# Performance work log

Measured on AMD Instinct MI355X. Metric: run time of the kernel, lower is better.

The kernel has to match this reference:

```python
import jax, jax.numpy as jnp
import numpy as np

INF = 1.0e10


def _embed(x, W1, b1, W2, b2):
    # TemplateAngleEmbedder: Linear -> GELU -> Linear
    return jax.nn.gelu(x @ W1 + b1) @ W2 + b2


def setup_inputs() -> dict:
    key = jax.random.key(0)
    ks = jax.random.split(key, 12)
    B, N, K = 2, 768, 30
    d_pair, d_msa, relpos_k = 128, 256, 32
    num_bins = 2 * relpos_k + 1  # 65
    s = 0.02
    # valid rigid frames: random rotations via QR (det fixed to +1) + translations
    A = jax.random.normal(ks[0], (B, N, 3, 3), dtype=jnp.float32)
    Q, _ = jnp.linalg.qr(A)
    Q = Q * jnp.sign(jnp.linalg.det(Q))[..., None, None]
    t = jax.random.normal(ks[1], (B, N, 3), dtype=jnp.float32) * 10.0
    frames = (jnp.zeros((B, N, 4, 4), dtype=jnp.float32)
              .at[..., :3, :3].set(Q)
              .at[..., :3, 3].set(t)
              .at[..., 3, 3].set(1.0))
    residue_index = jnp.tile(jnp.arange(N, dtype=jnp.int32)[None], (B, 1))
    return {
        'tf': jax.random.normal(ks[2], (B, N, 1), dtype=jnp.float32),
        'residue_index': residue_index,
        'true_frame_tensor': frames,
        'seq_mask': jnp.ones((B, N), dtype=jnp.float32),
        'W_tf': jax.random.normal(ks[3], (1, d_msa), dtype=jnp.float32) * s,
        'b_tf': jnp.zeros((d_msa,), dtype=jnp.float32),
        'Wa1': jax.random.normal(ks[4], (5, d_pair), dtype=jnp.float32) * s,
        'ba1': jnp.zeros((d_pair,), dtype=jnp.float32),
        'Wa2': jax.random.normal(ks[5], (d_pair, d_pair), dtype=jnp.float32) * s,
        'ba2': jnp.zeros((d_pair,), dtype=jnp.float32),
        'Wd1': jax.random.normal(ks[6], (3, d_pair), dtype=jnp.float32) * s,
        'bd1': jnp.zeros((d_pair,), dtype=jnp.float32),
        'Wd2': jax.random.normal(ks[7], (d_pair, d_pair), dtype=jnp.float32) * s,
        'bd2': jnp.zeros((d_pair,), dtype=jnp.float32),
        'W_rp': jax.random.normal(ks[8], (num_bins, d_pair), dtype=jnp.float32) * s,
        'b_rp': jnp.zeros((d_pair,), dtype=jnp.float32),
        'topk': 30,
    }


def _pair_features(true_frame_tensor, residue_index, seq_mask, topk):
    # get_pair_info: pairwise dist + masked topk KNN + gather + frame decompose
    B, N = residue_index.shape
    R = true_frame_tensor[..., :3, :3]          # [B,N,3,3]
    t = true_frame_tensor[..., :3, 3]           # [B,N,3]
    xyz = t[:, None, :, :] - t[:, :, None, :]   # [B,i,j,3] = t_j - t_i
    dist = jnp.linalg.norm(xyz, axis=-1)        # [B,N,N]
    eye = jnp.eye(N, dtype=bool)[None]          # [1,N,N]
    smask = seq_mask.astype(bool)
    pair_mask = smask[:, None, :] & smask[:, :, None]
    rel = residue_index[:, None, :] - residue_index[:, :, None]
    connect = jnp.abs(rel) == 1
    d4topk = jnp.where(eye, INF, dist)
    d4topk = jnp.where(pair_mask, d4topk, INF)
    d4topk = jnp.where(connect, -INF, d4topk)
    _, idx = jax.lax.top_k(-d4topk, topk)       # k smallest -> [B,N,K]
    topk_dist = jnp.take_along_axis(dist, idx, axis=-1)          # [B,N,K]
    knn_mask = jnp.take_along_axis(pair_mask & ~eye, idx, axis=-1)
    # gather neighbor frames and decompose into frame i's local coordinates:
    # t_rel = R_i^T (t_j - t_i)
    bidx = jnp.arange(B)[:, None, None]
    tj = t[bidx, idx]                            # [B,N,K,3]
    t_rel = jnp.einsum('bnxy,bnkx->bnky', R, tj - t[:, :, None, :])
    d = topk_dist[..., None]
    direct_angle = jnp.where(d > 0, t_rel / jnp.where(d > 0, d, 1.0), 0.0)
    eye_g = jnp.take_along_axis(jnp.broadcast_to(eye, (B, N, N)), idx, axis=-1)
    conn_g = jnp.take_along_axis(connect, idx, axis=-1)
    f32 = topk_dist.dtype
    ang_in = jnp.concatenate([eye_g[..., None].astype(f32),
                              conn_g[..., None].astype(f32),
                              direct_angle], axis=-1)            # [B,N,K,5]
    dst_in = jnp.concatenate([eye_g[..., None].astype(f32),
                              conn_g[..., None].astype(f32),
                              topk_dist[..., None]], axis=-1)    # [B,N,K,3]
    return ang_in, dst_in, knn_mask


def reference(tf, residue_index, true_frame_tensor, seq_mask,
              W_tf, b_tf, Wa1, ba1, Wa2, ba2, Wd1, bd1, Wd2, bd2,
              W_rp, b_rp, topk):
    relpos_k = (W_rp.shape[0] - 1) // 2
    # pair info computed under no_grad in the original
    ang_in, dst_in, _ = jax.lax.stop_gradient(
        _pair_features(true_frame_tensor, residue_index, seq_mask, topk))
    # tf is replaced by ones in the original forward
    ones_tf = jnp.ones_like(tf[..., :1])
    s = ones_tf @ W_tf + b_tf                                   # [B,N,d_msa]
    pair_rep_angle = _embed(ang_in, Wa1, ba1, Wa2, ba2)         # [B,N,K,d_pair]
    pair_rep_dist = _embed(dst_in, Wd1, bd1, Wd2, bd2)          # [B,N,K,d_pair]
    # relpos embedding (use_chain_relative=False)
    rp = residue_index[:, :, None] - residue_index[:, None, :]
    rp = jnp.clip(rp, -relpos_k, relpos_k) + relpos_k
    oh = jax.nn.one_hot(rp, W_rp.shape[0], dtype=W_rp.dtype)    # [B,N,N,65]
    relpos_emb = oh @ W_rp + b_rp                               # [B,N,N,d_pair]
    return (s, pair_rep_angle, pair_rep_dist, relpos_emb)
```

## Files before the change

kernel.cpp:

```cpp
#include <hip/hip_runtime.h>

typedef unsigned short u16;
typedef unsigned int   u32;
typedef unsigned long long u64;

typedef __attribute__((ext_vector_type(8))) short  short8;
typedef __attribute__((ext_vector_type(4))) float  floatx4;

__device__ __forceinline__ u16 f2bf(float f) {
    u32 u = __float_as_uint(f);
    u32 r = (u + 0x7FFFu + ((u >> 16) & 1u)) >> 16;
    return (u16)r;
}
__device__ __forceinline__ float bfu2f(u16 u) {
    union { u32 i; float f; } v; v.i = ((u32)u) << 16; return v.f;
}

constexpr int N     = 768;
constexpr int TOPK  = 30;
constexpr long OFF_ANG = 393216;
constexpr long OFF_DST = 6291456;
constexpr long OFF_RP  = 12189696;

__device__ __forceinline__ float dist_f32(float dx, float dy, float dz) {
    float s = __fadd_rn(__fadd_rn(__fmul_rn(dx, dx), __fmul_rn(dy, dy)), __fmul_rn(dz, dz));
    return __fsqrt_rn(s);
}

__global__ __launch_bounds__(256) void topk_feat_kernel(
    const float* __restrict__ frames, const int* __restrict__ resi,
    const float* __restrict__ smask, float* __restrict__ feat)
{
    __shared__ float s_t[N * 3];
    __shared__ float s_m[N];
    __shared__ int   s_r[N];
    int tid = threadIdx.x;
    int r0  = blockIdx.x * 4;
    int b   = r0 / N;
    for (int j = tid; j < N; j += 256) {
        s_r[j] = resi[b * N + j];
        s_m[j] = smask[b * N + j];
        long fb = (long)(b * N + j) * 16;
        s_t[j * 3 + 0] = frames[fb + 0 * 4 + 3];
        s_t[j * 3 + 1] = frames[fb + 1 * 4 + 3];
        s_t[j * 3 + 2] = frames[fb + 2 * 4 + 3];
    }
    __syncthreads();

    int wave = tid >> 6, lane = tid & 63;
    int r = r0 + wave;
    int i = r - b * N;
    float ti0 = s_t[i * 3], ti1 = s_t[i * 3 + 1], ti2 = s_t[i * 3 + 2];
    float mi = s_m[i];
    int   ri = s_r[i];

    u64 keys[12];
#pragma unroll
    for (int c = 0; c < 12; c++) {
        int j = lane + 64 * c;
        float dx = __fadd_rn(s_t[j * 3 + 0], -ti0);
        float dy = __fadd_rn(s_t[j * 3 + 1], -ti1);
        float dz = __fadd_rn(s_t[j * 3 + 2], -ti2);
        float dist = dist_f32(dx, dy, dz);
        int rd = s_r[j] - ri;
        bool conn = (rd == 1) || (rd == -1);
        bool bad  = (j == i) || (mi == 0.f) || (s_m[j] == 0.f);
        float d4 = conn ? -1e10f : (bad ? 1e10f : dist);
        u32 u = __float_as_uint(d4);
        u32 su = (u >> 31) ? ~u : (u | 0x80000000u);
        keys[c] = ((u64)su << 32) | (u32)j;
    }

    int my_j = 0;
    for (int k = 0; k < TOPK; k++) {
        u64 m = keys[0];
#pragma unroll
        for (int c = 1; c < 12; c++) m = m < keys[c] ? m : keys[c];
#pragma unroll
        for (int off = 32; off >= 1; off >>= 1) {
            u32 lo = (u32)m, hi = (u32)(m >> 32);
            u32 lo2 = __shfl_xor(lo, off);
            u32 hi2 = __shfl_xor(hi, off);
            u64 o = ((u64)hi2 << 32) | lo2;
            m = m < o ? m : o;
        }
#pragma unroll
        for (int c = 0; c < 12; c++) keys[c] = (keys[c] == m) ? ~0ull : keys[c];
        if (lane == k) my_j = (int)(m & 0xffffffffu);
    }

    if (lane < TOPK) {
        int j = my_j;
        float dx = __fadd_rn(s_t[j * 3 + 0], -ti0);
        float dy = __fadd_rn(s_t[j * 3 + 1], -ti1);
        float dz = __fadd_rn(s_t[j * 3 + 2], -ti2);
        float dist = dist_f32(dx, dy, dz);
        long fb = (long)(b * N + i) * 16;
        float R00 = frames[fb + 0], R01 = frames[fb + 1], R02 = frames[fb + 2];
        float R10 = frames[fb + 4], R11 = frames[fb + 5], R12 = frames[fb + 6];
        float R20 = frames[fb + 8], R21 = frames[fb + 9], R22 = frames[fb + 10];
        float t0 = R00 * dx + R10 * dy + R20 * dz;
        float t1 = R01 * dx + R11 * dy + R21 * dz;
        float t2 = R02 * dx + R12 * dy + R22 * dz;
        float a0 = dist > 0.f ? t0 / dist : 0.f;
        float a1 = dist > 0.f ? t1 / dist : 0.f;
        float a2 = dist > 0.f ? t2 / dist : 0.f;
        int rd = s_r[j] - ri;
        float conn = ((rd == 1) || (rd == -1)) ? 1.f : 0.f;
        float eye  = (j == i) ? 1.f : 0.f;
        long base = ((long)r * TOPK + lane) * 8;
        feat[base + 0] = eye; feat[base + 1] = conn;
        feat[base + 2] = a0;  feat[base + 3] = a1; feat[base + 4] = a2;
        feat[base + 5] = eye; feat[base + 6] = conn; feat[base + 7] = dist;
    }
}

template<int NF, int FOFF>
__device__ __forceinline__ void embed_body(
    int blk, const float* __restrict__ feat,
    const float* __restrict__ W1, const float* __restrict__ b1,
    const float* __restrict__ W2, const float* __restrict__ b2,
    float* __restrict__ out,
    u16* s_w2h, u16* s_w2l, float* s_w1, float* s_b1, float* s_b2)
{
    int tid = threadIdx.x;
    for (int e = tid; e < 128 * 128; e += 256) {
        int kk = e >> 7, nn = e & 127;
        float w  = W2[e];
        u16 hi = f2bf(w);
        float lo = __fadd_rn(w, -bfu2f(hi));
        s_w2h[nn * 136 + kk] = hi;
        s_w2l[nn * 136 + kk] = f2bf(lo);
    }
    for (int e = tid; e < NF * 128; e += 256) s_w1[e] = W1[e];
    if (tid < 128) { s_b1[tid] = b1[tid]; s_b2[tid] = b2[tid]; }
    __syncthreads();

    int wave = tid >> 6, lane = tid & 63;
    int m = lane & 15, q = lane >> 4;
    int row0 = blk * 64 + wave * 16;
    int row  = row0 + m;

    float f[NF];
#pragma unroll
    for (int t = 0; t < NF; t++) f[t] = feat[(long)row * 8 + FOFF + t];

    floatx4 acc[8];
#pragma unroll
    for (int nt = 0; nt < 8; nt++) acc[nt] = (floatx4){0.f, 0.f, 0.f, 0.f};

#pragma unroll
    for (int s = 0; s < 4; s++) {
        short8 ahi, alo;
#pragma unroll
        for (int jj = 0; jj < 8; jj++) {
            int kk = 32 * s + 8 * q + jj;
            float h = s_b1[kk];
#pragma unroll
            for (int t = 0; t < NF; t++) h += f[t] * s_w1[t * 128 + kk];
            float u  = 0.7978845608028654f * (h + 0.044715f * h * h * h);
            float e2 = __expf(-2.f * fabsf(u));
            float th = (1.f - e2) / (1.f + e2);
            th = u < 0.f ? -th : th;
            float g = 0.5f * h * (1.f + th);
            u16 ghi = f2bf(g);
            float glo = __fadd_rn(g, -bfu2f(ghi));
            ahi[jj] = (short)ghi;
            alo[jj] = (short)f2bf(glo);
        }
#pragma unroll
        for (int nt = 0; nt < 8; nt++) {
            int boff = (nt * 16 + m) * 136 + 32 * s + 8 * q;
            short8 bh = *(const short8*)&s_w2h[boff];
            short8 bl = *(const short8*)&s_w2l[boff];
            acc[nt] = __builtin_amdgcn_mfma_f32_16x16x32_bf16(ahi, bh, acc[nt], 0, 0, 0);
            acc[nt] = __builtin_amdgcn_mfma_f32_16x16x32_bf16(alo, bh, acc[nt], 0, 0, 0);
            acc[nt] = __builtin_amdgcn_mfma_f32_16x16x32_bf16(ahi, bl, acc[nt], 0, 0, 0);
        }
    }

#pragma unroll
    for (int nt = 0; nt < 8; nt++) {
#pragma unroll
        for (int rg = 0; rg < 4; rg++) {
            int rr = row0 + q * 4 + rg;
            int cc = nt * 16 + m;
            out[(long)rr * 128 + cc] = acc[nt][rg] + s_b2[cc];
        }
    }
}

__global__ __launch_bounds__(256) void fused_embed_s_kernel(
    const float* __restrict__ feat,
    const float* __restrict__ Wa1, const float* __restrict__ ba1,
    const float* __restrict__ Wa2, const float* __restrict__ ba2,
    const float* __restrict__ Wd1, const float* __restrict__ bd1,
    const float* __restrict__ Wd2, const float* __restrict__ bd2,
    const float* __restrict__ W_tf, const float* __restrict__ b_tf,
    float* __restrict__ out)
{
    __shared__ __align__(16) u16 s_w2h[128 * 136];
    __shared__ __align__(16) u16 s_w2l[128 * 136];
    __shared__ float s_w1[5 * 128];
    __shared__ float s_b1[128];
    __shared__ float s_b2[128];
    unsigned bx = blockIdx.x;
    if (bx < 720) {
        embed_body<5, 0>(bx, feat, Wa1, ba1, Wa2, ba2, out + OFF_ANG,
                         s_w2h, s_w2l, s_w1, s_b1, s_b2);
    } else if (bx < 1440) {
        embed_body<3, 5>(bx - 720, feat, Wd1, bd1, Wd2, bd2, out + OFF_DST,
                         s_w2h, s_w2l, s_w1, s_b1, s_b2);
    } else {
        int gid = (bx - 1440) * 256 + threadIdx.x;
        int c0  = (gid * 4) & 255;
        floatx4 o;
        o.x = W_tf[c0 + 0] + b_tf[c0 + 0];
        o.y = W_tf[c0 + 1] + b_tf[c0 + 1];
        o.z = W_tf[c0 + 2] + b_tf[c0 + 2];
        o.w = W_tf[c0 + 3] + b_tf[c0 + 3];
        *((floatx4*)out + gid) = o;
    }
}

__global__ __launch_bounds__(256) void relpos_kernel(
    const int* __restrict__ resi,
    const float* __restrict__ W_rp, const float* __restrict__ b_rp,
    float* __restrict__ out)
{
    int v   = blockIdx.x * 256 + threadIdx.x;
    int row = v >> 5, seg = v & 31;
    int b   = row >= N * N ? 1 : 0;
    int rem = row - b * (N * N);
    int i   = rem / N;
    int j   = rem - i * N;
    int d   = resi[b * N + i] - resi[b * N + j];
    d = d < -32 ? -32 : (d > 32 ? 32 : d);
    int bin = d + 32;
    floatx4 w  = ((const floatx4*)(W_rp + bin * 128))[seg];
    floatx4 bb = ((const floatx4*)b_rp)[seg];
    floatx4 o = w + bb;
    ((floatx4*)(out + OFF_RP))[v] = o;
}

extern "C" void kernel_launch(void* const* d_in, const int* in_sizes, int n_in,
                              void* d_out, int out_size, void* d_ws, size_t ws_size,
                              hipStream_t stream) {
    const int*   resi   = (const int*)d_in[1];
    const float* frames = (const float*)d_in[2];
    const float* smask  = (const float*)d_in[3];
    const float* W_tf   = (const float*)d_in[4];
    const float* b_tf   = (const float*)d_in[5];
    const float* Wa1    = (const float*)d_in[6];
    const float* ba1    = (const float*)d_in[7];
    const float* Wa2    = (const float*)d_in[8];
    const float* ba2    = (const float*)d_in[9];
    const float* Wd1    = (const float*)d_in[10];
    const float* bd1    = (const float*)d_in[11];
    const float* Wd2    = (const float*)d_in[12];
    const float* bd2    = (const float*)d_in[13];
    const float* W_rp   = (const float*)d_in[14];
    const float* b_rp   = (const float*)d_in[15];
    float* out  = (float*)d_out;
    float* feat = (float*)d_ws;

    hipLaunchKernelGGL(topk_feat_kernel, dim3(384), dim3(256), 0, stream,
                       frames, resi, smask, feat);
    hipLaunchKernelGGL(fused_embed_s_kernel, dim3(1824), dim3(256), 0, stream,
                       feat, Wa1, ba1, Wa2, ba2, Wd1, bd1, Wd2, bd2,
                       W_tf, b_tf, out);
    hipLaunchKernelGGL(relpos_kernel, dim3(147456), dim3(256), 0, stream,
                       resi, W_rp, b_rp, out);
}
```

Measured before the change: 717.7 us.

## Fuse relpos write into topk kernel with shared-memory bias-folded table

Merges the relpos embedding into the top-k feature kernel. The extra 1152 blocks each stage W_rp+b_rp and residue indices in shared memory, then stream 128 float4 writes per thread, replacing a 147456-block launch that read global weights per element. The relpos stores can overlap with the latency-bound top-k work and one launch is dropped. In exchange, shared memory per block grows to about 36KB for all blocks, which may lower occupancy of the top-k blocks.

```diff
diff --git a/kernel.cpp b/kernel.cpp
--- a/kernel.cpp
+++ b/kernel.cpp
@@ -27,91 +27,124 @@
     return __fsqrt_rn(s);
 }
 
-__global__ __launch_bounds__(256) void topk_feat_kernel(
+__global__ __launch_bounds__(256) void topk_relpos_kernel(
     const float* __restrict__ frames, const int* __restrict__ resi,
-    const float* __restrict__ smask, float* __restrict__ feat)
+    const float* __restrict__ smask, float* __restrict__ feat,
+    const float* __restrict__ W_rp, const float* __restrict__ b_rp,
+    float* __restrict__ out)
 {
-    __shared__ float s_t[N * 3];
-    __shared__ float s_m[N];
-    __shared__ int   s_r[N];
+    __shared__ __align__(16) char smem_raw[65 * 128 * 4 + N * 4];
     int tid = threadIdx.x;
-    int r0  = blockIdx.x * 4;
-    int b   = r0 / N;
-    for (int j = tid; j < N; j += 256) {
-        s_r[j] = resi[b * N + j];
-        s_m[j] = smask[b * N + j];
-        long fb = (long)(b * N + j) * 16;
-        s_t[j * 3 + 0] = frames[fb + 0 * 4 + 3];
-        s_t[j * 3 + 1] = frames[fb + 1 * 4 + 3];
-        s_t[j * 3 + 2] = frames[fb + 2 * 4 + 3];
-    }
-    __syncthreads();
-
-    int wave = tid >> 6, lane = tid & 63;
-    int r = r0 + wave;
-    int i = r - b * N;
-    float ti0 = s_t[i * 3], ti1 = s_t[i * 3 + 1], ti2 = s_t[i * 3 + 2];
-    float mi = s_m[i];
-    int   ri = s_r[i];
-
-    u64 keys[12];
-#pragma unroll
-    for (int c = 0; c < 12; c++) {
-        int j = lane + 64 * c;
-        float dx = __fadd_rn(s_t[j * 3 + 0], -ti0);
-        float dy = __fadd_rn(s_t[j * 3 + 1], -ti1);
-        float dz = __fadd_rn(s_t[j * 3 + 2], -ti2);
-        float dist = dist_f32(dx, dy, dz);
-        int rd = s_r[j] - ri;
-        bool conn = (rd == 1) || (rd == -1);
-        bool bad  = (j == i) || (mi == 0.f) || (s_m[j] == 0.f);
-        float d4 = conn ? -1e10f : (bad ? 1e10f : dist);
-        u32 u = __float_as_uint(d4);
-        u32 su = (u >> 31) ? ~u : (u | 0x80000000u);
-        keys[c] = ((u64)su << 32) | (u32)j;
-    }
-
-    int my_j = 0;
-    for (int k = 0; k < TOPK; k++) {
-        u64 m = keys[0];
-#pragma unroll
-        for (int c = 1; c < 12; c++) m = m < keys[c] ? m : keys[c];
-#pragma unroll
-        for (int off = 32; off >= 1; off >>= 1) {
-            u32 lo = (u32)m, hi = (u32)(m >> 32);
-            u32 lo2 = __shfl_xor(lo, off);
-            u32 hi2 = __shfl_xor(hi, off);
-            u64 o = ((u64)hi2 << 32) | lo2;
-            m = m < o ? m : o;
-        }
-#pragma unroll
-        for (int c = 0; c < 12; c++) keys[c] = (keys[c] == m) ? ~0ull : keys[c];
-        if (lane == k) my_j = (int)(m & 0xffffffffu);
-    }
-
-    if (lane < TOPK) {
-        int j = my_j;
-        float dx = __fadd_rn(s_t[j * 3 + 0], -ti0);
-        float dy = __fadd_rn(s_t[j * 3 + 1], -ti1);
-        float dz = __fadd_rn(s_t[j * 3 + 2], -ti2);
-        float dist = dist_f32(dx, dy, dz);
-        long fb = (long)(b * N + i) * 16;
-        float R00 = frames[fb + 0], R01 = frames[fb + 1], R02 = frames[fb + 2];
-        float R10 = frames[fb + 4], R11 = frames[fb + 5], R12 = frames[fb + 6];
-        float R20 = frames[fb + 8], R21 = frames[fb + 9], R22 = frames[fb + 10];
-        float t0 = R00 * dx + R10 * dy + R20 * dz;
-        float t1 = R01 * dx + R11 * dy + R21 * dz;
-        float t2 = R02 * dx + R12 * dy + R22 * dz;
-        float a0 = dist > 0.f ? t0 / dist : 0.f;
-        float a1 = dist > 0.f ? t1 / dist : 0.f;
-        float a2 = dist > 0.f ? t2 / dist : 0.f;
-        int rd = s_r[j] - ri;
-        float conn = ((rd == 1) || (rd == -1)) ? 1.f : 0.f;
-        float eye  = (j == i) ? 1.f : 0.f;
-        long base = ((long)r * TOPK + lane) * 8;
-        feat[base + 0] = eye; feat[base + 1] = conn;
-        feat[base + 2] = a0;  feat[base + 3] = a1; feat[base + 4] = a2;
-        feat[base + 5] = eye; feat[base + 6] = conn; feat[base + 7] = dist;
+
+    if (blockIdx.x < 384) {
+        float* s_t = (float*)smem_raw;
+        float* s_m = s_t + N * 3;
+        int*   s_r = (int*)(s_m + N);
+
+        int r0  = blockIdx.x * 4;
+        int b   = r0 / N;
+        for (int j = tid; j < N; j += 256) {
+            s_r[j] = resi[b * N + j];
+            s_m[j] = smask[b * N + j];
+            long fb = (long)(b * N + j) * 16;
+            s_t[j * 3 + 0] = frames[fb + 0 * 4 + 3];
+            s_t[j * 3 + 1] = frames[fb + 1 * 4 + 3];
+            s_t[j * 3 + 2] = frames[fb + 2 * 4 + 3];
+        }
+        __syncthreads();
+
+        int wave = tid >> 6, lane = tid & 63;
+        int r = r0 + wave;
+        int i = r - b * N;
+        float ti0 = s_t[i * 3], ti1 = s_t[i * 3 + 1], ti2 = s_t[i * 3 + 2];
+        float mi = s_m[i];
+        int   ri = s_r[i];
+
+        u64 keys[12];
+#pragma unroll
+        for (int c = 0; c < 12; c++) {
+            int j = lane + 64 * c;
+            float dx = __fadd_rn(s_t[j * 3 + 0], -ti0);
+            float dy = __fadd_rn(s_t[j * 3 + 1], -ti1);
+            float dz = __fadd_rn(s_t[j * 3 + 2], -ti2);
+            float dist = dist_f32(dx, dy, dz);
+            int rd = s_r[j] - ri;
+            bool conn = (rd == 1) || (rd == -1);
+            bool bad  = (j == i) || (mi == 0.f) || (s_m[j] == 0.f);
+            float d4 = conn ? -1e10f : (bad ? 1e10f : dist);
+            u32 u = __float_as_uint(d4);
+            u32 su = (u >> 31) ? ~u : (u | 0x80000000u);
+            keys[c] = ((u64)su << 32) | (u32)j;
+        }
+
+        int my_j = 0;
+        for (int k = 0; k < TOPK; k++) {
+            u64 m = keys[0];
+#pragma unroll
+            for (int c = 1; c < 12; c++) m = m < keys[c] ? m : keys[c];
+#pragma unroll
+            for (int off = 32; off >= 1; off >>= 1) {
+                u32 lo = (u32)m, hi = (u32)(m >> 32);
+                u32 lo2 = __shfl_xor(lo, off);
+                u32 hi2 = __shfl_xor(hi, off);
+                u64 o = ((u64)hi2 << 32) | lo2;
+                m = m < o ? m : o;
+            }
+#pragma unroll
+            for (int c = 0; c < 12; c++) keys[c] = (keys[c] == m) ? ~0ull : keys[c];
+            if (lane == k) my_j = (int)(m & 0xffffffffu);
+        }
+
+        if (lane < TOPK) {
+            int j = my_j;
+            float dx = __fadd_rn(s_t[j * 3 + 0], -ti0);
+            float dy = __fadd_rn(s_t[j * 3 + 1], -ti1);
+            float dz = __fadd_rn(s_t[j * 3 + 2], -ti2);
+            float dist = dist_f32(dx, dy, dz);
+            long fb = (long)(b * N + i) * 16;
+            float R00 = frames[fb + 0], R01 = frames[fb + 1], R02 = frames[fb + 2];
+            float R10 = frames[fb + 4], R11 = frames[fb + 5], R12 = frames[fb + 6];
+            float R20 = frames[fb + 8], R21 = frames[fb + 9], R22 = frames[fb + 10];
+            float t0 = R00 * dx + R10 * dy + R20 * dz;
+            float t1 = R01 * dx + R11 * dy + R21 * dz;
+            float t2 = R02 * dx + R12 * dy + R22 * dz;
+            float a0 = dist > 0.f ? t0 / dist : 0.f;
+            float a1 = dist > 0.f ? t1 / dist : 0.f;
+            float a2 = dist > 0.f ? t2 / dist : 0.f;
+            int rd = s_r[j] - ri;
+            float conn = ((rd == 1) || (rd == -1)) ? 1.f : 0.f;
+            float eye  = (j == i) ? 1.f : 0.f;
+            long base = ((long)r * TOPK + lane) * 8;
+            feat[base + 0] = eye; feat[base + 1] = conn;
+            feat[base + 2] = a0;  feat[base + 3] = a1; feat[base + 4] = a2;
+            feat[base + 5] = eye; feat[base + 6] = conn; feat[base + 7] = dist;
+        }
+    } else {
+        float* T   = (float*)smem_raw;
+        int*   s_r = (int*)(T + 65 * 128);
+
+        int blk = blockIdx.x - 384;
+        int b   = blk >= 576;
+
+        for (int e = tid; e < 65 * 128; e += 256) T[e] = W_rp[e] + b_rp[e & 127];
+        for (int j = tid; j < N; j += 256) s_r[j] = resi[b * N + j];
+        __syncthreads();
+
+        long vbase   = (long)blk << 15;
+        int  rowbase = (blk - b * 576) << 10;
+        floatx4* dst = (floatx4*)(out + OFF_RP) + vbase;
+
+#pragma unroll 4
+        for (int it = 0; it < 128; ++it) {
+            int lv  = (it << 8) + tid;
+            unsigned lrow = (unsigned)(rowbase + (lv >> 5));
+            int seg = lv & 31;
+            unsigned i = lrow / 768u;
+            unsigned j = lrow - i * 768u;
+            int d = s_r[i] - s_r[j];
+            d = d < -32 ? -32 : (d > 32 ? 32 : d);
+            dst[lv] = ((const floatx4*)(T + (unsigned)(d + 32) * 128))[seg];
+        }
     }
 }
 
@@ -223,26 +256,6 @@
     }
 }
 
-__global__ __launch_bounds__(256) void relpos_kernel(
-    const int* __restrict__ resi,
-    const float* __restrict__ W_rp, const float* __restrict__ b_rp,
-    float* __restrict__ out)
-{
-    int v   = blockIdx.x * 256 + threadIdx.x;
-    int row = v >> 5, seg = v & 31;
-    int b   = row >= N * N ? 1 : 0;
-    int rem = row - b * (N * N);
-    int i   = rem / N;
-    int j   = rem - i * N;
-    int d   = resi[b * N + i] - resi[b * N + j];
-    d = d < -32 ? -32 : (d > 32 ? 32 : d);
-    int bin = d + 32;
-    floatx4 w  = ((const floatx4*)(W_rp + bin * 128))[seg];
-    floatx4 bb = ((const floatx4*)b_rp)[seg];
-    floatx4 o = w + bb;
-    ((floatx4*)(out + OFF_RP))[v] = o;
-}
-
 extern "C" void kernel_launch(void* const* d_in, const int* in_sizes, int n_in,
                               void* d_out, int out_size, void* d_ws, size_t ws_size,
                               hipStream_t stream) {
@@ -264,11 +277,9 @@
     float* out  = (float*)d_out;
     float* feat = (float*)d_ws;
 
-    hipLaunchKernelGGL(topk_feat_kernel, dim3(384), dim3(256), 0, stream,
-                       frames, resi, smask, feat);
+    hipLaunchKernelGGL(topk_relpos_kernel, dim3(1536), dim3(256), 0, stream,
+                       frames, resi, smask, feat, W_rp, b_rp, out);
     hipLaunchKernelGGL(fused_embed_s_kernel, dim3(1824), dim3(256), 0, stream,
                        feat, Wa1, ba1, Wa2, ba2, Wd1, bd1, Wd2, bd2,
                        W_tf, b_tf, out);
-    hipLaunchKernelGGL(relpos_kernel, dim3(147456), dim3(256), 0, stream,
-                       resi, W_rp, b_rp, out);
-}
+}
```

Result: faster. 701.0 us (median of 2 runs) (-2.3%).
